# Optimization experiments

Hardware: AMD Instinct MI355X
Metric: run time of the kernel (lower is better)

The kernel has to match this reference:

```python
import jax, jax.numpy as jnp
import numpy as np

EPS = 1e-5      # BatchNorm1d eps
THETA = 1.0     # spike threshold
ALPHA = 5.0     # ATan surrogate alpha

@jax.custom_vjp
def atan_spike(x):
    # forward: heaviside; backward: ATan surrogate gradient
    return (x > 0).astype(x.dtype)

def _spike_fwd(x):
    return atan_spike(x), x

def _spike_bwd(x, g):
    return (g * ALPHA / (2.0 * (1.0 + (jnp.pi / 2.0 * ALPHA * x) ** 2)),)

atan_spike.defvjp(_spike_fwd, _spike_bwd)

def _lif_layer(x, W, beta_raw, gamma, bias, readout):
    # x: [T,B,J], W: [I,J]
    x = jnp.einsum('tbj,ij->tbi', x, W)
    # BatchNorm1d over (T*B) samples, per channel (training-mode batch stats)
    mean = jnp.mean(x, axis=(0, 1))
    var = jnp.var(x, axis=(0, 1))
    x = (x - mean) * jax.lax.rsqrt(var + EPS) * gamma + bias
    beta = jax.nn.sigmoid(beta_raw)
    B, I = x.shape[1], x.shape[2]
    U0 = jnp.zeros((B, I), x.dtype)
    if readout:
        def step(Ut, xt):
            Ut = beta * Ut + (1.0 - beta) * xt
            return Ut, Ut
        _, o = jax.lax.scan(step, U0, x)
    else:
        def step(carry, xt):
            Ut, St = carry
            Ut = beta * (Ut - THETA * St) + (1.0 - beta) * xt
            St = atan_spike(Ut - THETA)
            return (Ut, St), St
        _, o = jax.lax.scan(step, (U0, U0), x)
    return o  # [T,B,I]

def setup_inputs():
    key = jax.random.key(0)
    ks = jax.random.split(key, 8)
    B, T, J, H, O = 128, 512, 700, 512, 20
    def kaiming(k, out_dim, in_dim):
        # kaiming_uniform_(a=sqrt(5)) -> bound = 1/sqrt(fan_in)
        bound = 1.0 / np.sqrt(in_dim)
        return jax.random.uniform(k, (out_dim, in_dim), jnp.float32, -bound, bound)
    return {
        'x': jax.random.normal(ks[0], (B, T, J), jnp.float32),
        'W1': kaiming(ks[1], H, J),
        'beta1': jax.random.uniform(ks[2], (H,), jnp.float32, 0.0, 1.0),
        'g1': jnp.ones((H,), jnp.float32),
        'b1': jnp.zeros((H,), jnp.float32),
        'W2': kaiming(ks[3], H, H),
        'beta2': jax.random.uniform(ks[4], (H,), jnp.float32, 0.0, 1.0),
        'g2': jnp.ones((H,), jnp.float32),
        'b2': jnp.zeros((H,), jnp.float32),
        'Wr': kaiming(ks[5], O, H),
        'betar': jax.random.uniform(ks[6], (O,), jnp.float32, 0.0, 1.0),
        'gr': jnp.ones((O,), jnp.float32),
        'br': jnp.zeros((O,), jnp.float32),
    }

def reference(x, W1, beta1, g1, b1, W2, beta2, g2, b2, Wr, betar, gr, br):
    h = jnp.transpose(x, (1, 0, 2))  # [B,T,J] -> [T,B,J]
    h = _lif_layer(h, W1, beta1, g1, b1, readout=False)
    h = _lif_layer(h, W2, beta2, g2, b2, readout=False)
    h = _lif_layer(h, Wr, betar, gr, br, readout=True)
    p = jax.nn.softmax(h, axis=2)  # [T,B,O]
    return p.sum(axis=0)           # [B,O]
```

## Files before the change

kernel.cpp:

```cpp
#include <hip/hip_runtime.h>
#include <math.h>

typedef _Float16 f16_t;
typedef _Float16 f16x2 __attribute__((ext_vector_type(2)));
typedef _Float16 f16x8 __attribute__((ext_vector_type(8)));
typedef float f32x4 __attribute__((ext_vector_type(4)));

constexpr int Bn = 128;
constexpr int Tn = 512;
constexpr int Jn = 700;
constexpr int Jp = 704;
constexpr int Hn = 512;
constexpr int On = 20;
constexpr int Mn = Bn * Tn;

#define LDS_U32(p) ((__attribute__((address_space(3))) uint32_t*)(p))
#define GLB_U32(p) ((const __attribute__((address_space(1))) uint32_t*)(p))

template <int NT, bool SWZ>
__global__ __launch_bounds__(512, 4) void gemm_f16(
    const f16_t* __restrict__ A, const f16_t* __restrict__ W,
    float* __restrict__ C, float* __restrict__ s_out, float* __restrict__ q_out,
    int LDA, int LDW, int pairs, int Nout)
{
    constexpr int JT = 2 * NT;
    constexpr int NC = NT * 128;
    __shared__ __align__(16) f16_t sA[2 * 4096];
    __shared__ __align__(16) f16_t sW[2 * NT * 4096];

    int bx, by;
    if (SWZ) {
        const int g = blockIdx.x;
        by = (g >> 4) * 8 + (g & 7);
        bx = (g >> 3) & 1;
    } else {
        bx = blockIdx.x;
        by = blockIdx.y;
    }
    const int tid  = threadIdx.x;
    const int bm   = by * 128;
    const int bn   = bx * NC;
    const int lane = tid & 63;
    const int wv   = tid >> 6;
    const int wm   = (wv & 1) * 64;
    const int wn   = (wv >> 1) * (NT * 32);
    const int fr   = lane & 15;
    const int quad = lane >> 4;
    const int srow = lane >> 2;
    const int scol = (((lane & 3) ^ ((lane >> 3) & 3)) * 8);
    const int ksw  = ((quad ^ ((fr >> 1) & 3)) * 8);

    f32x4 acc[4][JT];
#pragma unroll
    for (int i = 0; i < 4; ++i)
#pragma unroll
        for (int j = 0; j < JT; ++j) acc[i][j] = {0.f, 0.f, 0.f, 0.f};

    for (int p = 0; p < pairs; ++p) {
#pragma unroll
        for (int cc = 0; cc < 2; ++cc) {
            const int c  = wv + cc * 8;
            const int s  = c >> 3;
            const int cr = (c & 7) * 16;
            const int kA = p * 64 + s * 32;
            const uint32_t off = __builtin_amdgcn_readfirstlane(s * 8192 + cr * 64);
            const f16_t* gp = A + (size_t)(bm + cr + srow) * LDA + kA + scol;
            __builtin_amdgcn_global_load_lds(GLB_U32(gp), LDS_U32((char*)sA + off), 16, 0, 0);
        }
#pragma unroll
        for (int cc = 0; cc < 2 * NT; ++cc) {
            const int c   = wv + cc * 8;
            const int h   = c / (NT * 8);
            const int rem = c % (NT * 8);
            const int nt  = rem >> 3;
            const int cr  = (rem & 7) * 16;
            const int kW  = p * 64 + h * 32;
            const uint32_t off = __builtin_amdgcn_readfirstlane((h * NT + nt) * 8192 + cr * 64);
            const f16_t* gp = W + (size_t)(bn + nt * 128 + cr + srow) * LDW + kW + scol;
            __builtin_amdgcn_global_load_lds(GLB_U32(gp), LDS_U32((char*)sW + off), 16, 0, 0);
        }
        __syncthreads();

#pragma unroll
        for (int h = 0; h < 2; ++h) {
            f16x8 av[4];
#pragma unroll
            for (int i = 0; i < 4; ++i)
                av[i] = *(const f16x8*)&sA[h * 4096 + (wm + i * 16 + fr) * 32 + ksw];
            f16x8 wf[JT];
#pragma unroll
            for (int jt = 0; jt < JT; ++jt) {
                const int n = wn + jt * 16 + fr;
                wf[jt] = *(const f16x8*)&sW[(h * NT + (n >> 7)) * 4096 + (n & 127) * 32 + ksw];
            }
#pragma unroll
            for (int i = 0; i < 4; ++i)
#pragma unroll
                for (int jt = 0; jt < JT; ++jt)
                    acc[i][jt] = __builtin_amdgcn_mfma_f32_16x16x32_f16(av[i], wf[jt], acc[i][jt], 0, 0, 0);
        }
        __syncthreads();
    }

    float* redS = (float*)sA;
    float* redQ = redS + 2 * NC;
#pragma unroll
    for (int jt = 0; jt < JT; ++jt) {
        const int gcol = bn + wn + jt * 16 + fr;
        float s = 0.f, q = 0.f;
        if (gcol < Nout) {
#pragma unroll
            for (int i = 0; i < 4; ++i) {
#pragma unroll
                for (int rg = 0; rg < 4; ++rg) {
                    const float v = acc[i][jt][rg];
                    C[(size_t)(bm + wm + i * 16 + quad * 4 + rg) * Nout + gcol] = v;
                    s += v;
                    q += v * v;
                }
            }
        }
        s += __shfl_xor(s, 16); s += __shfl_xor(s, 32);
        q += __shfl_xor(q, 16); q += __shfl_xor(q, 32);
        if (quad == 0) {
            const int lc = wn + jt * 16 + fr;
            redS[(wv & 1) * NC + lc] = s;
            redQ[(wv & 1) * NC + lc] = q;
        }
    }
    __syncthreads();
    if (tid < NC) {
        const int gcol = bn + tid;
        if (gcol < Nout) {
            atomicAdd(&s_out[gcol], redS[tid] + redS[NC + tid]);
            atomicAdd(&q_out[gcol], redQ[tid] + redQ[NC + tid]);
        }
    }
}

__global__ __launch_bounds__(512, 4) void gemm_narrow(
    const f16_t* __restrict__ A, const f16_t* __restrict__ W,
    float* __restrict__ C, float* __restrict__ s_out, float* __restrict__ q_out,
    int LDA, int LDW, int pairs, int Nout)
{
    __shared__ __align__(16) f16_t sA[2 * 4096];
    __shared__ __align__(16) f16_t sW[2 * 1024];

    const int tid  = threadIdx.x;
    const int bm   = blockIdx.x * 128;
    const int lane = tid & 63;
    const int wv   = tid >> 6;
    const int wm   = wv * 16;
    const int fr   = lane & 15;
    const int quad = lane >> 4;
    const int srow = lane >> 2;
    const int scol = (((lane & 3) ^ ((lane >> 3) & 3)) * 8);
    const int ksw  = ((quad ^ ((fr >> 1) & 3)) * 8);

    f32x4 acc[2];
    acc[0] = {0.f, 0.f, 0.f, 0.f};
    acc[1] = {0.f, 0.f, 0.f, 0.f};

    for (int p = 0; p < pairs; ++p) {
#pragma unroll
        for (int cc = 0; cc < 2; ++cc) {
            const int c  = wv + cc * 8;
            const int s  = c >> 3;
            const int cr = (c & 7) * 16;
            const int kA = p * 64 + s * 32;
            const uint32_t off = __builtin_amdgcn_readfirstlane(s * 8192 + cr * 64);
            const f16_t* gp = A + (size_t)(bm + cr + srow) * LDA + kA + scol;
            __builtin_amdgcn_global_load_lds(GLB_U32(gp), LDS_U32((char*)sA + off), 16, 0, 0);
        }
        if (wv < 4) {
            const int s  = wv >> 1;
            const int cr = (wv & 1) * 16;
            const int kW = p * 64 + s * 32;
            const uint32_t off = __builtin_amdgcn_readfirstlane(s * 2048 + cr * 64);
            const f16_t* gp = W + (size_t)(cr + srow) * LDW + kW + scol;
            __builtin_amdgcn_global_load_lds(GLB_U32(gp), LDS_U32((char*)sW + off), 16, 0, 0);
        }
        __syncthreads();

#pragma unroll
        for (int h = 0; h < 2; ++h) {
            const f16x8 av = *(const f16x8*)&sA[h * 4096 + (wm + fr) * 32 + ksw];
#pragma unroll
            for (int jt = 0; jt < 2; ++jt) {
                const f16x8 wf = *(const f16x8*)&sW[h * 1024 + (jt * 16 + fr) * 32 + ksw];
                acc[jt] = __builtin_amdgcn_mfma_f32_16x16x32_f16(av, wf, acc[jt], 0, 0, 0);
            }
        }
        __syncthreads();
    }

    float* redS = (float*)sA;
    float* redQ = redS + 256;
#pragma unroll
    for (int jt = 0; jt < 2; ++jt) {
        const int gcol = jt * 16 + fr;
        float s = 0.f, q = 0.f;
        if (gcol < Nout) {
#pragma unroll
            for (int rg = 0; rg < 4; ++rg) {
                const float v = acc[jt][rg];
                C[(size_t)(bm + wm + quad * 4 + rg) * Nout + gcol] = v;
                s += v;
                q += v * v;
            }
        }
        s += __shfl_xor(s, 16); s += __shfl_xor(s, 32);
        q += __shfl_xor(q, 16); q += __shfl_xor(q, 32);
        if (quad == 0) {
            redS[wv * 32 + gcol] = s;
            redQ[wv * 32 + gcol] = q;
        }
    }
    __syncthreads();
    if (tid < 32) {
        float ss = 0.f, qq = 0.f;
#pragma unroll
        for (int w = 0; w < 8; ++w) {
            ss += redS[w * 32 + tid];
            qq += redQ[w * 32 + tid];
        }
        if (tid < Nout) {
            atomicAdd(&s_out[tid], ss);
            atomicAdd(&q_out[tid], qq);
        }
    }
}

__global__ __launch_bounds__(256) void conv_x(const float* __restrict__ x,
                                              f16_t* __restrict__ A1) {
    const int idx = blockIdx.x * 256 + threadIdx.x;
    const int m = idx / 88, g = idx % 88;
    const int k8 = g * 8;
    const float* rp = x + (size_t)m * Jn + k8;
    float f[8];
    if (k8 + 8 <= Jn) {
        const float4 v0 = *(const float4*)rp;
        const float4 v1 = *(const float4*)(rp + 4);
        f[0] = v0.x; f[1] = v0.y; f[2] = v0.z; f[3] = v0.w;
        f[4] = v1.x; f[5] = v1.y; f[6] = v1.z; f[7] = v1.w;
    } else {
#pragma unroll
        for (int e = 0; e < 8; ++e) f[e] = (k8 + e < Jn) ? rp[e] : 0.f;
    }
    f16x8 hv;
#pragma unroll
    for (int e = 0; e < 8; ++e) hv[e] = (f16_t)f[e];
    *(f16x8*)&A1[(size_t)m * Jp + k8] = hv;
}

__global__ __launch_bounds__(256) void conv_w_all(const float* __restrict__ W1,
                                                  const float* __restrict__ W2,
                                                  const float* __restrict__ Wr,
                                                  f16_t* __restrict__ W1h,
                                                  f16_t* __restrict__ W2h,
                                                  f16_t* __restrict__ Wrh) {
    constexpr int n1 = Hn * (Jp / 8);
    constexpr int n2 = Hn * (Hn / 8);
    constexpr int n3 = 128 * (Hn / 8);
    int idx = blockIdx.x * 256 + threadIdx.x;
    const float* src; f16_t* dst; int N, K, KP;
    if (idx < n1)           { src = W1; dst = W1h; N = Hn;  K = Jn; KP = Jp; }
    else if (idx < n1 + n2) { src = W2; dst = W2h; N = Hn;  K = Hn; KP = Hn; idx -= n1; }
    else if (idx < n1 + n2 + n3) { src = Wr; dst = Wrh; N = On; K = Hn; KP = Hn; idx -= n1 + n2; }
    else return;
    const int n = idx / (KP / 8), g = idx % (KP / 8);
    const int k8 = g * 8;
    f16x8 hv;
#pragma unroll
    for (int e = 0; e < 8; ++e) {
        const float f = (n < N && k8 + e < K) ? src[(size_t)n * K + k8 + e] : 0.f;
        hv[e] = (f16_t)f;
    }
    *(f16x8*)&dst[(size_t)n * KP + k8] = hv;
}

__global__ __launch_bounds__(256) void lif_scan(const float* __restrict__ X,
                                                f16_t* __restrict__ S_out,
                                                const float* __restrict__ sums,
                                                const float* __restrict__ sumsq,
                                                const float* __restrict__ beta_raw,
                                                const float* __restrict__ gamma,
                                                const float* __restrict__ bias) {
    const int gid = blockIdx.x * 256 + threadIdx.x;
    const int b  = gid >> 8;
    const int cq = gid & 255;
    const int i0 = cq * 2;

    float g[2], bi[2], bt[2], ob[2];
#pragma unroll
    for (int e = 0; e < 2; ++e) {
        const int i = i0 + e;
        const float invM = 1.f / (float)Mn;
        const float mean = sums[i] * invM;
        const float var  = sumsq[i] * invM - mean * mean;
        const float inv  = rsqrtf(var + 1e-5f);
        g[e]  = gamma[i] * inv;
        bi[e] = bias[i] - mean * g[e];
        bt[e] = 1.f / (1.f + expf(-beta_raw[i]));
        ob[e] = 1.f - bt[e];
    }

    const float2* Xp = (const float2*)(X + (size_t)b * Tn * Hn) + cq;
    f16x2* Sp2 = (f16x2*)(S_out + (size_t)b * Tn * Hn) + cq;

    float U[2] = {0.f, 0.f}, Sp[2] = {0.f, 0.f};
#pragma unroll 8
    for (int t = 0; t < Tn; ++t) {
        const float2 v = Xp[(size_t)t * (Hn / 2)];
        const float vf[2] = {v.x, v.y};
        f16x2 so;
#pragma unroll
        for (int e = 0; e < 2; ++e) {
            const float xt = vf[e] * g[e] + bi[e];
            U[e] = bt[e] * (U[e] - Sp[e]) + ob[e] * xt;
            Sp[e] = (U[e] > 1.0f) ? 1.0f : 0.0f;
            so[e] = (f16_t)Sp[e];
        }
        Sp2[(size_t)t * (Hn / 2)] = so;
    }
}

__global__ __launch_bounds__(256) void readout_kernel(const float* __restrict__ A,
                                                      const float* __restrict__ sums,
                                                      const float* __restrict__ sumsq,
                                                      const float* __restrict__ beta_raw,
                                                      const float* __restrict__ gamma,
                                                      const float* __restrict__ bias,
                                                      float* __restrict__ out) {
    __shared__ float xs[Tn * On];
    __shared__ float gsh[On], bsh[On], betash[On];
    __shared__ float red[4][On];

    const int b = blockIdx.x;
    const int tid = threadIdx.x;

    if (tid < On) {
        const float invM = 1.f / (float)Mn;
        const float mean = sums[tid] * invM;
        const float var = sumsq[tid] * invM - mean * mean;
        const float inv = rsqrtf(var + 1e-5f);
        const float g = gamma[tid] * inv;
        gsh[tid] = g;
        bsh[tid] = bias[tid] - mean * g;
        betash[tid] = 1.f / (1.f + expf(-beta_raw[tid]));
    }
    __syncthreads();

    const float* Ab = A + (size_t)b * Tn * On;
    for (int idx = tid; idx < Tn * On; idx += 256) {
        const int o = idx % On;
        xs[idx] = Ab[idx] * gsh[o] + bsh[o];
    }
    __syncthreads();

    if (tid < On) {
        const float beta = betash[tid], omb = 1.f - beta;
        float U = 0.f;
        for (int t = 0; t < Tn; ++t) {
            U = beta * U + omb * xs[t * On + tid];
            xs[t * On + tid] = U;
        }
    }
    __syncthreads();

    float part[On];
#pragma unroll
    for (int o = 0; o < On; ++o) part[o] = 0.f;

    for (int t = tid; t < Tn; t += 256) {
        float v[On];
        float m = -1e30f;
#pragma unroll
        for (int o = 0; o < On; ++o) {
            v[o] = xs[t * On + o];
            m = fmaxf(m, v[o]);
        }
        float s = 0.f;
#pragma unroll
        for (int o = 0; o < On; ++o) {
            v[o] = expf(v[o] - m);
            s += v[o];
        }
        const float rs = 1.f / s;
#pragma unroll
        for (int o = 0; o < On; ++o) part[o] += v[o] * rs;
    }

#pragma unroll
    for (int o = 0; o < On; ++o) {
#pragma unroll
        for (int off = 32; off > 0; off >>= 1) part[o] += __shfl_down(part[o], off);
    }
    const int lane = tid & 63, wid = tid >> 6;
    if (lane == 0) {
#pragma unroll
        for (int o = 0; o < On; ++o) red[wid][o] = part[o];
    }
    __syncthreads();
    if (tid < On) out[b * On + tid] = red[0][tid] + red[1][tid] + red[2][tid] + red[3][tid];
}

extern "C" void kernel_launch(void* const* d_in, const int* in_sizes, int n_in,
                              void* d_out, int out_size, void* d_ws, size_t ws_size,
                              hipStream_t stream) {
    const float* x   = (const float*)d_in[0];
    const float* W1  = (const float*)d_in[1];
    const float* be1 = (const float*)d_in[2];
    const float* g1  = (const float*)d_in[3];
    const float* b1  = (const float*)d_in[4];
    const float* W2  = (const float*)d_in[5];
    const float* be2 = (const float*)d_in[6];
    const float* b2g = (const float*)d_in[7];
    const float* b2  = (const float*)d_in[8];
    const float* Wr  = (const float*)d_in[9];
    const float* ber = (const float*)d_in[10];
    const float* gr  = (const float*)d_in[11];
    const float* br  = (const float*)d_in[12];
    float* out = (float*)d_out;

    char* ws = (char*)d_ws;
    const size_t r0Bytes   = (size_t)Mn * Jp * sizeof(f16_t);
    const size_t bufCBytes = (size_t)Mn * Hn * sizeof(float);
    f16_t* A1   = (f16_t*)ws;
    f16_t* bufS = (f16_t*)ws;
    float* bufC = (float*)(ws + r0Bytes);
    char*  p    = ws + r0Bytes + bufCBytes;
    float* bufR = (float*)p;              p += (size_t)Mn * On * sizeof(float);
    f16_t* W1h  = (f16_t*)p;              p += (size_t)Hn * Jp * sizeof(f16_t);
    f16_t* W2h  = (f16_t*)p;              p += (size_t)Hn * Hn * sizeof(f16_t);
    f16_t* Wrh  = (f16_t*)p;              p += (size_t)128 * Hn * sizeof(f16_t);
    float* stats = (float*)p;
    float* s1 = stats;       float* q1 = s1 + Hn;
    float* s2 = q1 + Hn;     float* q2 = s2 + Hn;
    float* s3 = q2 + Hn;     float* q3 = s3 + 32;

    hipMemsetAsync(stats, 0, (4 * Hn + 64) * sizeof(float), stream);

    conv_x<<<(Mn * 88) / 256, 256, 0, stream>>>(x, A1);
    conv_w_all<<<(Hn * 88 + Hn * 64 + 128 * 64 + 255) / 256, 256, 0, stream>>>(
        W1, W2, Wr, W1h, W2h, Wrh);

    gemm_f16<2, true><<<2 * (Mn / 128), 512, 0, stream>>>(A1, W1h, bufC, s1, q1,
        Jp, Jp, Jp / 64, Hn);
    lif_scan<<<(Bn * Hn / 2) / 256, 256, 0, stream>>>(bufC, bufS, s1, q1, be1, g1, b1);

    gemm_f16<2, true><<<2 * (Mn / 128), 512, 0, stream>>>(bufS, W2h, bufC, s2, q2,
        Hn, Hn, Hn / 64, Hn);
    lif_scan<<<(Bn * Hn / 2) / 256, 256, 0, stream>>>(bufC, bufS, s2, q2, be2, b2g, b2);

    gemm_narrow<<<Mn / 128, 512, 0, stream>>>(bufS, Wrh, bufR, s3, q3,
        Hn, Hn, Hn / 64, On);
    readout_kernel<<<Bn, 256, 0, stream>>>(bufR, s3, q3, ber, gr, br, out);
}
```

Before: 524.1 us.

## Double-buffer GEMM LDS tiles and shrink N-tile to 128 columns

Adds a two-stage LDS double buffer to the f16 MFMA GEMM. The next K-slab is issued via global_load_lds before computing the current one, with explicit vmcnt waits and raw barriers, so global loads overlap with MFMA work. It also halves the per-block N tile (NT=2 to NT=1) and quadruples the grid with an adjusted swizzle, giving more blocks and fewer accumulators per block. The cost is more A-tile reloads across column blocks, doubled LDS per block, and reliance on hand-written waitcnt correctness.

```diff
diff --git a/kernel.cpp b/kernel.cpp
--- a/kernel.cpp
+++ b/kernel.cpp
@@ -25,14 +25,14 @@
 {
     constexpr int JT = 2 * NT;
     constexpr int NC = NT * 128;
-    __shared__ __align__(16) f16_t sA[2 * 4096];
-    __shared__ __align__(16) f16_t sW[2 * NT * 4096];
+    __shared__ __align__(16) f16_t sA[2 * 2 * 4096];
+    __shared__ __align__(16) f16_t sW[2 * 2 * NT * 4096];
 
     int bx, by;
     if (SWZ) {
         const int g = blockIdx.x;
-        by = (g >> 4) * 8 + (g & 7);
-        bx = (g >> 3) & 1;
+        by = (g >> 5) * 8 + (g & 7);
+        bx = (g >> 3) & 3;
     } else {
         bx = blockIdx.x;
         by = blockIdx.y;
@@ -56,14 +56,15 @@
 #pragma unroll
         for (int j = 0; j < JT; ++j) acc[i][j] = {0.f, 0.f, 0.f, 0.f};
 
-    for (int p = 0; p < pairs; ++p) {
+    auto stage = [&](int buf, int p) {
 #pragma unroll
         for (int cc = 0; cc < 2; ++cc) {
             const int c  = wv + cc * 8;
             const int s  = c >> 3;
             const int cr = (c & 7) * 16;
             const int kA = p * 64 + s * 32;
-            const uint32_t off = __builtin_amdgcn_readfirstlane(s * 8192 + cr * 64);
+            const uint32_t off =
+                __builtin_amdgcn_readfirstlane(buf * 16384 + s * 8192 + cr * 64);
             const f16_t* gp = A + (size_t)(bm + cr + srow) * LDA + kA + scol;
             __builtin_amdgcn_global_load_lds(GLB_U32(gp), LDS_U32((char*)sA + off), 16, 0, 0);
         }
@@ -75,23 +76,38 @@
             const int nt  = rem >> 3;
             const int cr  = (rem & 7) * 16;
             const int kW  = p * 64 + h * 32;
-            const uint32_t off = __builtin_amdgcn_readfirstlane((h * NT + nt) * 8192 + cr * 64);
+            const uint32_t off = __builtin_amdgcn_readfirstlane(
+                buf * (NT * 16384) + (h * NT + nt) * 8192 + cr * 64);
             const f16_t* gp = W + (size_t)(bn + nt * 128 + cr + srow) * LDW + kW + scol;
             __builtin_amdgcn_global_load_lds(GLB_U32(gp), LDS_U32((char*)sW + off), 16, 0, 0);
         }
-        __syncthreads();
-
+    };
+
+    stage(0, 0);
+    int cur = 0;
+    for (int p = 0; p < pairs; ++p) {
+        if (p + 1 < pairs) {
+            stage(cur ^ 1, p + 1);
+            asm volatile("s_waitcnt vmcnt(%0)" :: "i"(2 + 2 * NT) : "memory");
+        } else {
+            asm volatile("s_waitcnt vmcnt(0)" ::: "memory");
+        }
+        __builtin_amdgcn_s_barrier();
+        __builtin_amdgcn_sched_barrier(0);
+
+        const int aBase = cur * 8192;
+        const int wBase = cur * (NT * 8192);
 #pragma unroll
         for (int h = 0; h < 2; ++h) {
             f16x8 av[4];
 #pragma unroll
             for (int i = 0; i < 4; ++i)
-                av[i] = *(const f16x8*)&sA[h * 4096 + (wm + i * 16 + fr) * 32 + ksw];
+                av[i] = *(const f16x8*)&sA[aBase + h * 4096 + (wm + i * 16 + fr) * 32 + ksw];
             f16x8 wf[JT];
 #pragma unroll
             for (int jt = 0; jt < JT; ++jt) {
                 const int n = wn + jt * 16 + fr;
-                wf[jt] = *(const f16x8*)&sW[(h * NT + (n >> 7)) * 4096 + (n & 127) * 32 + ksw];
+                wf[jt] = *(const f16x8*)&sW[wBase + (h * NT + (n >> 7)) * 4096 + (n & 127) * 32 + ksw];
             }
 #pragma unroll
             for (int i = 0; i < 4; ++i)
@@ -99,7 +115,11 @@
                 for (int jt = 0; jt < JT; ++jt)
                     acc[i][jt] = __builtin_amdgcn_mfma_f32_16x16x32_f16(av[i], wf[jt], acc[i][jt], 0, 0, 0);
         }
-        __syncthreads();
+
+        asm volatile("s_waitcnt lgkmcnt(0)" ::: "memory");
+        __builtin_amdgcn_s_barrier();
+        __builtin_amdgcn_sched_barrier(0);
+        cur ^= 1;
     }
 
     float* redS = (float*)sA;
@@ -445,11 +465,11 @@
     conv_w_all<<<(Hn * 88 + Hn * 64 + 128 * 64 + 255) / 256, 256, 0, stream>>>(
         W1, W2, Wr, W1h, W2h, Wrh);
 
-    gemm_f16<2, true><<<2 * (Mn / 128), 512, 0, stream>>>(A1, W1h, bufC, s1, q1,
+    gemm_f16<1, true><<<4 * (Mn / 128), 512, 0, stream>>>(A1, W1h, bufC, s1, q1,
         Jp, Jp, Jp / 64, Hn);
     lif_scan<<<(Bn * Hn / 2) / 256, 256, 0, stream>>>(bufC, bufS, s1, q1, be1, g1, b1);
 
-    gemm_f16<2, true><<<2 * (Mn / 128), 512, 0, stream>>>(bufS, W2h, bufC, s2, q2,
+    gemm_f16<1, true><<<4 * (Mn / 128), 512, 0, stream>>>(bufS, W2h, bufC, s2, q2,
         Hn, Hn, Hn / 64, Hn);
     lif_scan<<<(Bn * Hn / 2) / 256, 256, 0, stream>>>(bufC, bufS, s2, q2, be2, b2g, b2);
 
```

New measurement: 537.6 us. +2.6%, slower.
